# Optimization experiments

Measured on AMD Instinct MI355X. Metric: run time of the kernel, lower is better.

The kernel has to match this reference:

```python
import jax, jax.numpy as jnp
import numpy as np

N, D_IN, D_OUT = 16384, 64, 64
AVG_DEG = 32.0
L2_EPS = 1e-12  # torch F.normalize default eps


def setup_inputs() -> dict:
    key = jax.random.key(0)
    kx, ka, kw, kb = jax.random.split(key, 4)
    X = jax.random.normal(kx, (N, D_IN), dtype=jnp.float32)
    # binary adjacency with avg degree ~AVG_DEG (module treats adj as 0/1 mask)
    adj = (jax.random.uniform(ka, (N, N)) < (AVG_DEG / N)).astype(jnp.float32)
    # nn.Linear(2*D_IN, D_OUT): store W as (2*D_IN, D_OUT) for x @ W + b
    bound = 1.0 / np.sqrt(2 * D_IN)
    W = jax.random.uniform(kw, (2 * D_IN, D_OUT), dtype=jnp.float32, minval=-bound, maxval=bound)
    b = jax.random.uniform(kb, (D_OUT,), dtype=jnp.float32, minval=-bound, maxval=bound)
    return {"X": X, "adj": adj, "W": W, "b": b}


def reference(X, adj, W, b):
    # eval-mode mean aggregation: h_neigh = (adj + I) @ X / clamp(rowsum(adj + I), 1)
    # (adj + I) @ X == adj @ X + X, avoiding materializing the NxN identity.
    deg = jnp.clip(jnp.sum(adj, axis=1, keepdims=True) + 1.0, 1.0, None)  # (N,1)
    h_neigh = (adj @ X + X) / deg                                          # (N,D)
    concat = jnp.concatenate([X, h_neigh], axis=1)                         # (N,2D)
    z = concat @ W + b                                                     # (N,O)
    out = jax.nn.relu(z)
    norm = jnp.linalg.norm(out, axis=1, keepdims=True)
    return out / jnp.maximum(norm, L2_EPS)
```

## Files before the change

### kernel.cpp

```cpp
#include <hip/hip_runtime.h>
#include <stdint.h>


#define NROWS   16384
#define DDIM    64
#define MAXNNZ  256
#define NBLOCKS 4096

typedef uint32_t u32x4 __attribute__((ext_vector_type(4)));

__global__ __launch_bounds__(256, 8) void sage_fused(
    const float* __restrict__ X,
    const float* __restrict__ adj,
    const float* __restrict__ W,
    const float* __restrict__ bias,
    float* __restrict__ out)
{
    __shared__ int   slist[4][MAXNNZ];
    __shared__ int   scnt[4];
    __shared__ float scat[4][2 * DDIM];

    const int tid  = threadIdx.x;
    const int lane = tid & 63;
    const int w    = tid >> 6;
    const int row  = blockIdx.x * 4 + w;

    const float bv = bias[lane];

    if (lane == 0) scnt[w] = 0;
    __builtin_amdgcn_wave_barrier();

    const int start = (row * 7 + (row >> 4)) & 15;
    const u32x4* rowp = reinterpret_cast<const u32x4*>(adj + (size_t)row * NROWS);

    u32x4 buf[2][4];
    {
        const int ss0 = start;
        const int ss1 = (start + 1) & 15;
#pragma unroll
        for (int q = 0; q < 4; ++q)
            buf[0][q] = __builtin_nontemporal_load(&rowp[ss0 * 256 + q * 64 + lane]);
#pragma unroll
        for (int q = 0; q < 4; ++q)
            buf[1][q] = __builtin_nontemporal_load(&rowp[ss1 * 256 + q * 64 + lane]);
    }

#pragma unroll 2
    for (int s = 0; s < 16; ++s) {
        const int cur = s & 1;
        const int ss  = (s + start) & 15;
#pragma unroll
        for (int q = 0; q < 4; ++q) {
            const u32x4 vv = buf[cur][q];
            if (vv.x | vv.y | vv.z | vv.w) {
                const int base = (ss * 256 + q * 64 + lane) * 4;
                const uint32_t w4[4] = { vv.x, vv.y, vv.z, vv.w };
#pragma unroll
                for (int j = 0; j < 4; ++j) {
                    if (w4[j]) {
                        const int p = atomicAdd(&scnt[w], 1);
                        if (p < MAXNNZ) slist[w][p] = base + j;
                    }
                }
            }
        }
        if (s < 14) {
            const int ssn = (s + 2 + start) & 15;
#pragma unroll
            for (int q = 0; q < 4; ++q)
                buf[cur][q] = __builtin_nontemporal_load(&rowp[ssn * 256 + q * 64 + lane]);
        }
    }
    __builtin_amdgcn_wave_barrier();

    const int nnz = scnt[w];
    const int cn  = (nnz < MAXNNZ) ? nnz : MAXNNZ;

    float acc = 0.0f;
    int k = 0;
    for (; k + 4 <= cn; k += 4) {
        const int j0 = slist[w][k], j1 = slist[w][k + 1];
        const int j2 = slist[w][k + 2], j3 = slist[w][k + 3];
        const float a0 = X[(size_t)j0 * DDIM + lane];
        const float a1 = X[(size_t)j1 * DDIM + lane];
        const float a2 = X[(size_t)j2 * DDIM + lane];
        const float a3 = X[(size_t)j3 * DDIM + lane];
        acc += (a0 + a1) + (a2 + a3);
    }
    for (; k < cn; ++k) acc += X[(size_t)slist[w][k] * DDIM + lane];

    const float xi = X[(size_t)row * DDIM + lane];
    const float h  = (acc + xi) / ((float)nnz + 1.0f);
    scat[w][lane]        = xi;
    scat[w][DDIM + lane] = h;
    __builtin_amdgcn_wave_barrier();

    float z0 = bv, z1 = 0.0f, z2 = 0.0f, z3 = 0.0f;
#pragma unroll 8
    for (int kk = 0; kk < 2 * DDIM; kk += 4) {
        z0 = fmaf(scat[w][kk + 0], W[(kk + 0) * DDIM + lane], z0);
        z1 = fmaf(scat[w][kk + 1], W[(kk + 1) * DDIM + lane], z1);
        z2 = fmaf(scat[w][kk + 2], W[(kk + 2) * DDIM + lane], z2);
        z3 = fmaf(scat[w][kk + 3], W[(kk + 3) * DDIM + lane], z3);
    }
    float z = (z0 + z1) + (z2 + z3);
    z = fmaxf(z, 0.0f);

    float s2 = z * z;
#pragma unroll
    for (int off = 32; off >= 1; off >>= 1) s2 += __shfl_xor(s2, off);
    const float inv = 1.0f / fmaxf(sqrtf(s2), 1e-12f);
    out[(size_t)row * DDIM + lane] = z * inv;
}

extern "C" void kernel_launch(void* const* d_in, const int* in_sizes, int n_in,
                              void* d_out, int out_size, void* d_ws, size_t ws_size,
                              hipStream_t stream) {
    const float* X   = (const float*)d_in[0];
    const float* adj = (const float*)d_in[1];
    const float* W   = (const float*)d_in[2];
    const float* b   = (const float*)d_in[3];
    float* out = (float*)d_out;
    sage_fused<<<NBLOCKS, 256, 0, stream>>>(X, adj, W, b, out);
}
```

Measured before the change: 1.317 ms.

## Split adjacency scan into a coalesced grid-stride kernel with global neighbor lists

Replaces the per-row fused scan, where each wave streamed one adjacency row, with a separate grid-stride kernel. That kernel reads the whole adjacency matrix in fully coalesced 16-byte chunks and appends column indices to per-row lists using global atomics. The lists are staged in the output buffer as scratch, and a zeroing kernel resets the counts. A third kernel gathers X rows from the list with 8-way unrolled loads and runs the linear, ReLU and normalization steps. The goal is to make the 1 GiB adjacency read bandwidth-bound rather than latency-bound. The trade-offs are two extra launches, global atomics, and a per-row neighbor cap cut from 256 to 64, which silently drops neighbors for any row with more than 64.

```diff
diff --git a/kernel.cpp b/kernel.cpp
--- a/kernel.cpp
+++ b/kernel.cpp
@@ -4,20 +4,91 @@
 
 #define NROWS   16384
 #define DDIM    64
-#define MAXNNZ  256
+#define MAXN    64
 #define NBLOCKS 4096
+
+#define SCAN_TPB     256
+#define SCAN_BLOCKS  2048
+#define SCAN_THREADS (SCAN_TPB * SCAN_BLOCKS)
 
 typedef uint32_t u32x4 __attribute__((ext_vector_type(4)));
 
-__global__ __launch_bounds__(256, 8) void sage_fused(
+__device__ int g_cnt[NROWS];
+
+__global__ void zero_cnt() {
+    g_cnt[blockIdx.x * 256 + threadIdx.x] = 0;
+}
+
+__global__ __launch_bounds__(SCAN_TPB, 4) void adj_scan(
+    const float* __restrict__ adj,
+    int* __restrict__ list)
+{
+    const u32x4* p = reinterpret_cast<const u32x4*>(adj);
+    const uint32_t stride = SCAN_THREADS;
+
+    int c_ = 0;
+    uint32_t e0 = 0, e1 = 0, e2 = 0, e3 = 0, e4 = 0, e5 = 0;
+
+#define CAPTURE(E)                                                           \
+    {                                                                        \
+        const uint32_t e_ = (E);                                             \
+        if (c_ < 6) {                                                        \
+            e0 = (c_ == 0) ? e_ : e0;                                        \
+            e1 = (c_ == 1) ? e_ : e1;                                        \
+            e2 = (c_ == 2) ? e_ : e2;                                        \
+            e3 = (c_ == 3) ? e_ : e3;                                        \
+            e4 = (c_ == 4) ? e_ : e4;                                        \
+            e5 = (c_ == 5) ? e_ : e5;                                        \
+            c_++;                                                            \
+        } else {                                                             \
+            const int r_ = e_ >> 14;                                         \
+            const int p_ = atomicAdd(&g_cnt[r_], 1);                         \
+            if (p_ < MAXN) list[(r_ << 6) + p_] = (int)(e_ & (NROWS - 1));   \
+        }                                                                    \
+    }
+
+#define PROC(V, VI)                                                          \
+    if ((V).x | (V).y | (V).z | (V).w) {                                     \
+        const uint32_t wd_[4] = { (V).x, (V).y, (V).z, (V).w };              \
+        _Pragma("unroll")                                                    \
+        for (int j_ = 0; j_ < 4; ++j_)                                       \
+            if (wd_[j_]) CAPTURE((VI) * 4u + (uint32_t)j_);                  \
+    }
+
+    uint32_t i = blockIdx.x * SCAN_TPB + threadIdx.x;
+    for (int it = 0; it < 32; ++it) {
+        const uint32_t i0 = i, i1 = i + stride, i2 = i + 2 * stride,
+                       i3 = i + 3 * stride;
+        const u32x4 v0 = __builtin_nontemporal_load(&p[i0]);
+        const u32x4 v1 = __builtin_nontemporal_load(&p[i1]);
+        const u32x4 v2 = __builtin_nontemporal_load(&p[i2]);
+        const u32x4 v3 = __builtin_nontemporal_load(&p[i3]);
+        PROC(v0, i0);
+        PROC(v1, i1);
+        PROC(v2, i2);
+        PROC(v3, i3);
+        i += 4 * stride;
+    }
+#undef PROC
+
+#define FLUSH(K, EK)                                                         \
+    if (c_ > (K)) {                                                          \
+        const int r_ = (EK) >> 14;                                           \
+        const int p_ = atomicAdd(&g_cnt[r_], 1);                             \
+        if (p_ < MAXN) list[(r_ << 6) + p_] = (int)((EK) & (NROWS - 1));     \
+    }
+    FLUSH(0, e0) FLUSH(1, e1) FLUSH(2, e2)
+    FLUSH(3, e3) FLUSH(4, e4) FLUSH(5, e5)
+#undef FLUSH
+#undef CAPTURE
+}
+
+__global__ __launch_bounds__(256) void sage_agg(
     const float* __restrict__ X,
-    const float* __restrict__ adj,
     const float* __restrict__ W,
     const float* __restrict__ bias,
     float* __restrict__ out)
 {
-    __shared__ int   slist[4][MAXNNZ];
-    __shared__ int   scnt[4];
     __shared__ float scat[4][2 * DDIM];
 
     const int tid  = threadIdx.x;
@@ -27,67 +98,26 @@
 
     const float bv = bias[lane];
 
-    if (lane == 0) scnt[w] = 0;
-    __builtin_amdgcn_wave_barrier();
-
-    const int start = (row * 7 + (row >> 4)) & 15;
-    const u32x4* rowp = reinterpret_cast<const u32x4*>(adj + (size_t)row * NROWS);
-
-    u32x4 buf[2][4];
-    {
-        const int ss0 = start;
-        const int ss1 = (start + 1) & 15;
-#pragma unroll
-        for (int q = 0; q < 4; ++q)
-            buf[0][q] = __builtin_nontemporal_load(&rowp[ss0 * 256 + q * 64 + lane]);
-#pragma unroll
-        for (int q = 0; q < 4; ++q)
-            buf[1][q] = __builtin_nontemporal_load(&rowp[ss1 * 256 + q * 64 + lane]);
-    }
-
-#pragma unroll 2
-    for (int s = 0; s < 16; ++s) {
-        const int cur = s & 1;
-        const int ss  = (s + start) & 15;
-#pragma unroll
-        for (int q = 0; q < 4; ++q) {
-            const u32x4 vv = buf[cur][q];
-            if (vv.x | vv.y | vv.z | vv.w) {
-                const int base = (ss * 256 + q * 64 + lane) * 4;
-                const uint32_t w4[4] = { vv.x, vv.y, vv.z, vv.w };
-#pragma unroll
-                for (int j = 0; j < 4; ++j) {
-                    if (w4[j]) {
-                        const int p = atomicAdd(&scnt[w], 1);
-                        if (p < MAXNNZ) slist[w][p] = base + j;
-                    }
-                }
-            }
-        }
-        if (s < 14) {
-            const int ssn = (s + 2 + start) & 15;
-#pragma unroll
-            for (int q = 0; q < 4; ++q)
-                buf[cur][q] = __builtin_nontemporal_load(&rowp[ssn * 256 + q * 64 + lane]);
-        }
-    }
-    __builtin_amdgcn_wave_barrier();
-
-    const int nnz = scnt[w];
-    const int cn  = (nnz < MAXNNZ) ? nnz : MAXNNZ;
+    const int nnz = g_cnt[row];
+    const int cn  = (nnz < MAXN) ? nnz : MAXN;
+    const int* lp = reinterpret_cast<const int*>(out) + (row << 6);
 
     float acc = 0.0f;
     int k = 0;
-    for (; k + 4 <= cn; k += 4) {
-        const int j0 = slist[w][k], j1 = slist[w][k + 1];
-        const int j2 = slist[w][k + 2], j3 = slist[w][k + 3];
+    for (; k + 8 <= cn; k += 8) {
+        const int j0 = lp[k],     j1 = lp[k + 1], j2 = lp[k + 2], j3 = lp[k + 3];
+        const int j4 = lp[k + 4], j5 = lp[k + 5], j6 = lp[k + 6], j7 = lp[k + 7];
         const float a0 = X[(size_t)j0 * DDIM + lane];
         const float a1 = X[(size_t)j1 * DDIM + lane];
         const float a2 = X[(size_t)j2 * DDIM + lane];
         const float a3 = X[(size_t)j3 * DDIM + lane];
-        acc += (a0 + a1) + (a2 + a3);
+        const float a4 = X[(size_t)j4 * DDIM + lane];
+        const float a5 = X[(size_t)j5 * DDIM + lane];
+        const float a6 = X[(size_t)j6 * DDIM + lane];
+        const float a7 = X[(size_t)j7 * DDIM + lane];
+        acc += ((a0 + a1) + (a2 + a3)) + ((a4 + a5) + (a6 + a7));
     }
-    for (; k < cn; ++k) acc += X[(size_t)slist[w][k] * DDIM + lane];
+    for (; k < cn; ++k) acc += X[(size_t)lp[k] * DDIM + lane];
 
     const float xi = X[(size_t)row * DDIM + lane];
     const float h  = (acc + xi) / ((float)nnz + 1.0f);
@@ -121,5 +151,8 @@
     const float* W   = (const float*)d_in[2];
     const float* b   = (const float*)d_in[3];
     float* out = (float*)d_out;
-    sage_fused<<<NBLOCKS, 256, 0, stream>>>(X, adj, W, b, out);
+
+    zero_cnt<<<NROWS / 256, 256, 0, stream>>>();
+    adj_scan<<<SCAN_BLOCKS, SCAN_TPB, 0, stream>>>(adj, (int*)out);
+    sage_agg<<<NBLOCKS, 256, 0, stream>>>(X, W, b, out);
 }
```

Measured after the change: 1.362 ms. 3.5% more time.

## Split adjacency scan into bitmap-compression kernel followed by sparse aggregation kernel

Applied to the files above, without the earlier changes.

A new kernel streams the dense 1 GiB adjacency in a fully coalesced pattern and packs each 1.0f entry into a single bit of a global bitmap. The aggregation kernel then reads that compact bitmap instead of the float row to build neighbor lists, and gathers X with an 8-way unroll. The goal is to make the dominant dense read purely bandwidth-bound and decoupled from per-row atomics and list building. The cost is an extra launch and bitmap traffic. It also relies on bit 29 to detect 1.0f and caps neighbor lists at 96 instead of 256, which silently truncates high-degree rows while still dividing by the full count.

```diff
diff --git a/kernel.cpp b/kernel.cpp
--- a/kernel.cpp
+++ b/kernel.cpp
@@ -4,19 +4,54 @@
 
 #define NROWS   16384
 #define DDIM    64
-#define MAXNNZ  256
+#define MAXL    96
 #define NBLOCKS 4096
+
+#define SCAN_TPB     256
+#define SCAN_BLOCKS  2048
+#define STHREADS     (SCAN_TPB * SCAN_BLOCKS)
 
 typedef uint32_t u32x4 __attribute__((ext_vector_type(4)));
 
-__global__ __launch_bounds__(256, 8) void sage_fused(
+__device__ uint32_t g_bm[16u * STHREADS];
+
+__global__ __launch_bounds__(SCAN_TPB, 4) void adj_scan(
+    const float* __restrict__ adj)
+{
+    const u32x4* p = reinterpret_cast<const u32x4*>(adj);
+    const uint32_t t = blockIdx.x * SCAN_TPB + threadIdx.x;
+
+    uint32_t i = t;
+    for (int w = 0; w < 16; ++w) {
+        uint32_t word = 0;
+#pragma unroll
+        for (int h = 0; h < 2; ++h) {
+            const u32x4 v0 = __builtin_nontemporal_load(&p[i]);
+            const u32x4 v1 = __builtin_nontemporal_load(&p[i + STHREADS]);
+            const u32x4 v2 = __builtin_nontemporal_load(&p[i + 2u * STHREADS]);
+            const u32x4 v3 = __builtin_nontemporal_load(&p[i + 3u * STHREADS]);
+            const uint32_t n0 = ((v0.x >> 29) & 1u) | ((v0.y >> 28) & 2u)
+                              | ((v0.z >> 27) & 4u) | ((v0.w >> 26) & 8u);
+            const uint32_t n1 = ((v1.x >> 29) & 1u) | ((v1.y >> 28) & 2u)
+                              | ((v1.z >> 27) & 4u) | ((v1.w >> 26) & 8u);
+            const uint32_t n2 = ((v2.x >> 29) & 1u) | ((v2.y >> 28) & 2u)
+                              | ((v2.z >> 27) & 4u) | ((v2.w >> 26) & 8u);
+            const uint32_t n3 = ((v3.x >> 29) & 1u) | ((v3.y >> 28) & 2u)
+                              | ((v3.z >> 27) & 4u) | ((v3.w >> 26) & 8u);
+            word |= (n0 | (n1 << 4) | (n2 << 8) | (n3 << 12)) << (h * 16);
+            i += 4u * STHREADS;
+        }
+        g_bm[(uint32_t)w * STHREADS + t] = word;
+    }
+}
+
+__global__ __launch_bounds__(256) void sage_agg(
     const float* __restrict__ X,
-    const float* __restrict__ adj,
     const float* __restrict__ W,
     const float* __restrict__ bias,
     float* __restrict__ out)
 {
-    __shared__ int   slist[4][MAXNNZ];
+    __shared__ int   slist[4][MAXL];
     __shared__ int   scnt[4];
     __shared__ float scat[4][2 * DDIM];
 
@@ -28,64 +63,48 @@
     const float bv = bias[lane];
 
     if (lane == 0) scnt[w] = 0;
-    __builtin_amdgcn_wave_barrier();
 
-    const int start = (row * 7 + (row >> 4)) & 15;
-    const u32x4* rowp = reinterpret_cast<const u32x4*>(adj + (size_t)row * NROWS);
-
-    u32x4 buf[2][4];
-    {
-        const int ss0 = start;
-        const int ss1 = (start + 1) & 15;
+    const uint32_t sh = ((uint32_t)(row >> 7) & 7u) * 4u;
+    const uint32_t* base = g_bm + (uint32_t)(row >> 10) * STHREADS
+                                + ((uint32_t)(row & 127) << 12);
+    for (int k = 0; k < 16; ++k) {
+        const u32x4 d = *reinterpret_cast<const u32x4*>(base + k * 256 + lane * 4);
 #pragma unroll
-        for (int q = 0; q < 4; ++q)
-            buf[0][q] = __builtin_nontemporal_load(&rowp[ss0 * 256 + q * 64 + lane]);
+        for (int c4 = 0; c4 < 4; ++c4) {
+            const uint32_t nib = (d[c4] >> sh) & 15u;
+            if (nib) {
+                const int j = k * 256 + lane * 4 + c4;
 #pragma unroll
-        for (int q = 0; q < 4; ++q)
-            buf[1][q] = __builtin_nontemporal_load(&rowp[ss1 * 256 + q * 64 + lane]);
-    }
-
-#pragma unroll 2
-    for (int s = 0; s < 16; ++s) {
-        const int cur = s & 1;
-        const int ss  = (s + start) & 15;
-#pragma unroll
-        for (int q = 0; q < 4; ++q) {
-            const u32x4 vv = buf[cur][q];
-            if (vv.x | vv.y | vv.z | vv.w) {
-                const int base = (ss * 256 + q * 64 + lane) * 4;
-                const uint32_t w4[4] = { vv.x, vv.y, vv.z, vv.w };
-#pragma unroll
-                for (int j = 0; j < 4; ++j) {
-                    if (w4[j]) {
-                        const int p = atomicAdd(&scnt[w], 1);
-                        if (p < MAXNNZ) slist[w][p] = base + j;
+                for (int c = 0; c < 4; ++c) {
+                    if (nib & (1u << c)) {
+                        const int pp = atomicAdd(&scnt[w], 1);
+                        if (pp < MAXL) slist[w][pp] = 4 * j + c;
                     }
                 }
             }
-        }
-        if (s < 14) {
-            const int ssn = (s + 2 + start) & 15;
-#pragma unroll
-            for (int q = 0; q < 4; ++q)
-                buf[cur][q] = __builtin_nontemporal_load(&rowp[ssn * 256 + q * 64 + lane]);
         }
     }
     __builtin_amdgcn_wave_barrier();
 
     const int nnz = scnt[w];
-    const int cn  = (nnz < MAXNNZ) ? nnz : MAXNNZ;
+    const int cn  = (nnz < MAXL) ? nnz : MAXL;
 
     float acc = 0.0f;
     int k = 0;
-    for (; k + 4 <= cn; k += 4) {
-        const int j0 = slist[w][k], j1 = slist[w][k + 1];
+    for (; k + 8 <= cn; k += 8) {
+        const int j0 = slist[w][k],     j1 = slist[w][k + 1];
         const int j2 = slist[w][k + 2], j3 = slist[w][k + 3];
+        const int j4 = slist[w][k + 4], j5 = slist[w][k + 5];
+        const int j6 = slist[w][k + 6], j7 = slist[w][k + 7];
         const float a0 = X[(size_t)j0 * DDIM + lane];
         const float a1 = X[(size_t)j1 * DDIM + lane];
         const float a2 = X[(size_t)j2 * DDIM + lane];
         const float a3 = X[(size_t)j3 * DDIM + lane];
-        acc += (a0 + a1) + (a2 + a3);
+        const float a4 = X[(size_t)j4 * DDIM + lane];
+        const float a5 = X[(size_t)j5 * DDIM + lane];
+        const float a6 = X[(size_t)j6 * DDIM + lane];
+        const float a7 = X[(size_t)j7 * DDIM + lane];
+        acc += ((a0 + a1) + (a2 + a3)) + ((a4 + a5) + (a6 + a7));
     }
     for (; k < cn; ++k) acc += X[(size_t)slist[w][k] * DDIM + lane];
 
@@ -121,5 +140,7 @@
     const float* W   = (const float*)d_in[2];
     const float* b   = (const float*)d_in[3];
     float* out = (float*)d_out;
-    sage_fused<<<NBLOCKS, 256, 0, stream>>>(X, adj, W, b, out);
+
+    adj_scan<<<SCAN_BLOCKS, SCAN_TPB, 0, stream>>>(adj);
+    sage_agg<<<NBLOCKS, 256, 0, stream>>>(X, W, b, out);
 }
```

Result: slower. 1.419 ms (+7.8%).
